# Kernel tuning notes

Measured on AMD Instinct MI355X. Metric: run time of the kernel, lower is better.

## Reference

```python
import jax, jax.numpy as jnp
import numpy as np

B, CIN, COUT, RES, WDIM, K, GRID = 2, 512, 512, 256, 512, 3, 8
W_COORD_DIST, W_LERP_MULT = 2.0, 1.0
LRELU_SLOPE = 0.2
ACT_GAIN = float(np.sqrt(2.0))  # bias_act def_gain for lrelu
PAD = K // 2  # force_zero_padding=False -> padding = kernel_size//2


def setup_inputs() -> dict:
    key = jax.random.key(0)
    ks = jax.random.split(key, 8)
    return {
        "x": jax.random.normal(ks[0], (B, CIN, RES, RES), jnp.float32),
        "w": jax.random.normal(ks[1], (B, WDIM), jnp.float32),
        "w_context": jax.random.normal(ks[2], (B, 2, WDIM), jnp.float32),
        "weight": jax.random.normal(ks[3], (COUT, CIN, K, K), jnp.float32),
        "affine_w": jax.random.normal(ks[4], (CIN, WDIM), jnp.float32),
        "affine_b": jnp.ones((CIN,), jnp.float32),  # bias_init=1
        "bias": jnp.zeros((COUT,), jnp.float32),
        "noise_strength": jnp.float32(0.1),  # nonzero so noise path is active
        "noise_raw": jax.random.normal(ks[5], (B, 1, RES, RES), jnp.float32),
        "left_borders_idx": jax.random.randint(ks[6], (B,), 0, GRID),
    }


def _to_patches(x):
    # [b,c,h,w] -> [b*grid, c, h, w/grid], matching view/permute order in patchwise_op
    b, c, h, w = x.shape
    wp = w // GRID
    return x.reshape(b, c, h, GRID, wp).transpose(0, 3, 1, 2, 4).reshape(b * GRID, c, h, wp)


def _from_patches(y, b):
    bg, c, h, wp = y.shape
    return y.reshape(b, GRID, c, h, wp).transpose(0, 2, 3, 1, 4).reshape(b, c, h, GRID * wp)


def _style_lerp(x, styles, left_borders_idx):
    # fast_manual_bilinear_mult_row: width-wise piecewise-linear interpolation of
    # 3 style anchors (left ctx, center, right ctx); center anchor sits at the
    # column given by left_borders_idx (in patch units); anchor spacing = w*w_coord_dist/2.
    b, c, h, w = x.shape
    patch = w // GRID
    D = w * W_COORD_DIST / 2.0
    cols = jnp.arange(w, dtype=x.dtype) + 0.5  # [w]
    center = left_borders_idx.astype(x.dtype)[:, None] * patch  # [b,1]
    t = jnp.clip((cols[None, :] - center) / D * W_LERP_MULT, -1.0, 1.0)  # [b,w]
    a = jnp.clip(-t, 0.0, 1.0)   # weight on left-context style
    r = jnp.clip(t, 0.0, 1.0)    # weight on right-context style
    m = 1.0 - a - r              # weight on center style
    scol = (a[..., None] * styles[:, 0][:, None, :]
            + m[..., None] * styles[:, 1][:, None, :]
            + r[..., None] * styles[:, 2][:, None, :])  # [b,w,c]
    return x * scol.transpose(0, 2, 1)[:, :, None, :]  # broadcast over h


def reference(x, w, w_context, weight, affine_w, affine_b, bias, noise_strength, noise_raw, left_borders_idx):
    b = x.shape[0]
    # run_spatial_affine: FullyConnectedLayer with weight_gain 1/sqrt(w_dim)
    wg = jnp.stack([w_context[:, 0], w, w_context[:, 1]], axis=1)  # [b,3,wdim]
    styles = jnp.einsum('bsd,cd->bsc', wg, affine_w) * (1.0 / np.sqrt(WDIM)) + affine_b  # [b,3,cin]

    # per-patch instance norm (unbiased std over (h, w_patch)), h > grid*2 holds
    wp = RES // GRID
    xp = x.reshape(b, CIN, RES, GRID, wp)
    std = jnp.std(xp, axis=(2, 4), keepdims=True, ddof=1)
    x = (xp / (std + 1e-8)).reshape(b, CIN, RES, RES)

    # style modulation
    x = _style_lerp(x, styles, left_borders_idx)

    # patchwise conv2d (up=1, flip_weight=True -> plain cross-correlation, pad k//2)
    xpat = _to_patches(x)
    y = jax.lax.conv_general_dilated(
        xpat, weight, window_strides=(1, 1), padding=((PAD, PAD), (PAD, PAD)),
        dimension_numbers=('NCHW', 'OIHW', 'NCHW'))
    x = _from_patches(y, b)

    # demodulation + noise fma
    demod = jax.lax.rsqrt(jnp.sum(weight * weight, axis=(1, 2, 3)) + 1e-8)  # [cout]
    x = x * demod[None, :, None, None] + noise_raw * noise_strength

    # bias_act: lrelu(x+b) * def_gain (gain=1, no clamp)
    x = x + bias[None, :, None, None]
    return jnp.where(x >= 0, x, x * LRELU_SLOPE) * ACT_GAIN
```

## Files before the change

### kernel.cpp

```cpp
#include <hip/hip_runtime.h>
#include <hip/hip_bf16.h>

#define BATCH 2
#define CIN 512
#define COUT 512
#define RES 256
#define WDIM 512
#define GRIDP 8
#define PW 32
#define NPATCH 16
#define LRELU 0.2f
#define ACT_GAIN 1.41421356237309515f

typedef __attribute__((ext_vector_type(8))) short bf16x8;
typedef __attribute__((ext_vector_type(4))) float f32x4;

#define SZ_XMOD (134217728ULL)
#define OFF_WBF (SZ_XMOD)
#define SZ_WBF  (9ULL*512*512*2)
#define OFF_STYLES (OFF_WBF + SZ_WBF)
#define SZ_STYLES (2*3*512*4)
#define OFF_INVSTD (OFF_STYLES + SZ_STYLES)
#define SZ_INVSTD (2*512*8*4)
#define OFF_DEMOD (OFF_INVSTD + SZ_INVSTD)

__global__ void k_styles(const float* __restrict__ w, const float* __restrict__ wctx,
                         const float* __restrict__ affw, const float* __restrict__ affb,
                         float* __restrict__ styles) {
    int tid = blockIdx.x * 256 + threadIdx.x;
    if (tid >= BATCH * 3 * CIN) return;
    int c = tid & 511;
    int s = (tid >> 9) % 3;
    int b = tid / (3 * 512);
    const float* row = (s == 0) ? (wctx + b * 2 * WDIM)
                     : (s == 1) ? (w + b * WDIM)
                                : (wctx + b * 2 * WDIM + WDIM);
    const float* aw = affw + (size_t)c * WDIM;
    float acc = 0.f;
    for (int d = 0; d < WDIM; ++d) acc += row[d] * aw[d];
    styles[tid] = acc * 0.044194173824159216f + affb[c];
}

__global__ void k_wprep(const float* __restrict__ weight, __hip_bfloat16* __restrict__ wbf,
                        float* __restrict__ demod) {
    int o = blockIdx.x;
    int t = threadIdx.x;
    const float* wrow = weight + (size_t)o * 4608;
    float ss = 0.f;
    for (int i = t; i < 4608; i += 256) { float v = wrow[i]; ss += v * v; }
    #pragma unroll
    for (int off = 32; off; off >>= 1) ss += __shfl_down(ss, off, 64);
    __shared__ float red[4];
    if ((t & 63) == 0) red[t >> 6] = ss;
    __syncthreads();
    if (t == 0) {
        float tot = red[0] + red[1] + red[2] + red[3];
        demod[o] = 1.0f / sqrtf(tot + 1e-8f);
    }
    for (int k = 0; k < 9; ++k)
        for (int ci = t; ci < 512; ci += 256)
            wbf[(size_t)k * COUT * CIN + (size_t)o * CIN + ci] = __float2bfloat16(wrow[ci * 9 + k]);
}

__global__ void k_std(const float* __restrict__ x, float* __restrict__ inv_std) {
    int bid = blockIdx.x;
    int g = bid & 7;
    int c = (bid >> 3) & 511;
    int b = bid >> 12;
    const float* base = x + ((size_t)(b * 512 + c) * 256) * 256 + g * 32;
    int t = threadIdx.x;
    float s = 0.f, ss = 0.f;
    #pragma unroll 4
    for (int i = 0; i < 32; ++i) {
        int e = t + (i << 8);
        int h = e >> 5, wp = e & 31;
        float v = base[h * 256 + wp];
        s += v; ss += v * v;
    }
    #pragma unroll
    for (int off = 32; off; off >>= 1) {
        s += __shfl_down(s, off, 64);
        ss += __shfl_down(ss, off, 64);
    }
    __shared__ float rs[4], rss[4];
    if ((t & 63) == 0) { rs[t >> 6] = s; rss[t >> 6] = ss; }
    __syncthreads();
    if (t == 0) {
        float S = rs[0] + rs[1] + rs[2] + rs[3];
        float SS = rss[0] + rss[1] + rss[2] + rss[3];
        float var = (SS - S * S * (1.f / 8192.f)) * (1.f / 8191.f);
        var = fmaxf(var, 0.f);
        inv_std[bid] = 1.f / (sqrtf(var) + 1e-8f);
    }
}

__global__ void k_normmod(const float* __restrict__ x, const float* __restrict__ styles,
                          const float* __restrict__ inv_std, const int* __restrict__ lbi,
                          __hip_bfloat16* __restrict__ xmod) {
    int bid = blockIdx.x;
    int ht = bid & 31;
    int cc = (bid >> 5) & 7;
    int p = bid >> 8;
    int b = p >> 3, g = p & 7;
    int t = threadIdx.x;
    __shared__ float st[3][64];
    __shared__ float istd[64];
    __shared__ __align__(16) __hip_bfloat16 tile[8 * 33 * 66];
    if (t < 192) {
        int s = t / 64, c = t % 64;
        st[s][c] = styles[(b * 3 + s) * 512 + cc * 64 + c];
    } else {
        int c = t - 192;
        istd[c] = inv_std[(b * 512 + cc * 64 + c) * 8 + g];
    }
    __syncthreads();
    float center = (float)(lbi[b] * PW);
    const float* xb = x + ((size_t)(b * 512 + cc * 64) * 256 + ht * 8) * 256 + g * 32;
    #pragma unroll 4
    for (int i = 0; i < 16; ++i) {
        int cell = t + (i << 8);
        int c = cell >> 6;
        int rem = cell & 63;
        int h = rem >> 3;
        int v4 = rem & 7;
        float4 xv = *(const float4*)(xb + ((size_t)c * 256 + h) * 256 + v4 * 4);
        float sc = istd[c];
        float s0 = st[0][c], s1 = st[1][c], s2 = st[2][c];
        float colb = (float)(g * 32 + v4 * 4) + 0.5f;
        const float* xvp = &xv.x;
        #pragma unroll
        for (int k = 0; k < 4; ++k) {
            float tc = (colb + (float)k - center) * 0.00390625f;
            tc = fminf(fmaxf(tc, -1.f), 1.f);
            float a = fmaxf(-tc, 0.f), r = fmaxf(tc, 0.f);
            float m = 1.f - a - r;
            float scol = a * s0 + m * s1 + r * s2;
            tile[(h * 33 + (v4 * 4 + k)) * 66 + c] = __float2bfloat16(xvp[k] * sc * scol);
        }
    }
    __syncthreads();
    __hip_bfloat16* ob = xmod + (size_t)(p * 256 + ht * 8) * 32 * 512 + cc * 64;
    #pragma unroll 4
    for (int i = 0; i < 8; ++i) {
        int cell = t + (i << 8);
        int c8 = cell & 7;
        int wp = (cell >> 3) & 31;
        int h = cell >> 8;
        const __hip_bfloat16* src = tile + (h * 33 + wp) * 66 + c8 * 8;
        uint4 v;
        v.x = *(const unsigned*)(src);
        v.y = *(const unsigned*)(src + 2);
        v.z = *(const unsigned*)(src + 4);
        v.w = *(const unsigned*)(src + 6);
        *(uint4*)(ob + (size_t)(h * 32 + wp) * 512 + c8 * 8) = v;
    }
}

__global__ void __launch_bounds__(256, 2)
k_conv(const __hip_bfloat16* __restrict__ xmod, const __hip_bfloat16* __restrict__ wbf,
       const float* __restrict__ demod, const float* __restrict__ bias,
       const float* __restrict__ noise, const float* __restrict__ nstr_p,
       float* __restrict__ out) {
    int ht = blockIdx.x;
    int p = blockIdx.y;
    int mb = blockIdx.z;
    int b = p >> 3, g = p & 7;
    int cout0 = mb * 128;
    int h0b = ht * 4;
    int t = threadIdx.x;
    int lane = t & 63, wid = t >> 6;
    int wm = wid >> 1, wn = wid & 1;
    int l15 = lane & 15, q = lane >> 4;

    __shared__ __align__(16) __hip_bfloat16 wsA[3 * 128 * 32];
    __shared__ __align__(16) __hip_bfloat16 xsB[4 * 6 * 34 * 8];

    f32x4 acc[4][4];
    #pragma unroll
    for (int i = 0; i < 4; ++i)
        #pragma unroll
        for (int j = 0; j < 4; ++j) acc[i][j] = (f32x4){0.f, 0.f, 0.f, 0.f};

    const __hip_bfloat16* xpat = xmod + (size_t)p * 256 * 32 * 512;

    for (int cin0 = 0; cin0 < 512; cin0 += 32) {
        __syncthreads();
        for (int idx = t; idx < 816; idx += 256) {
            int k8 = idx / 204;
            int rem = idx - k8 * 204;
            int hs = rem / 34;
            int wps = rem - hs * 34;
            int hg = h0b + hs - 1;
            uint4 v = make_uint4(0u, 0u, 0u, 0u);
            if (wps >= 1 && wps <= 32 && hg >= 0 && hg < 256)
                v = *(const uint4*)(xpat + (size_t)(hg * 32 + (wps - 1)) * 512 + cin0 + k8 * 8);
            *(uint4*)(xsB + ((k8 * 6 + hs) * 34 + wps) * 8) = v;
        }
        for (int kh = 0; kh < 3; ++kh) {
            __syncthreads();
            for (int idx = t; idx < 1536; idx += 256) {
                int kw = idx >> 9;
                int r = (idx >> 2) & 127;
                int k8 = idx & 3;
                uint4 v = *(const uint4*)(wbf + (size_t)((kh * 3 + kw) * 512 + cout0 + r) * 512 + cin0 + k8 * 8);
                *(uint4*)(wsA + ((kw * 128 + r) * 32 + k8 * 8)) = v;
            }
            __syncthreads();
            #pragma unroll
            for (int kw = 0; kw < 3; ++kw) {
                bf16x8 af[4], bfr[4];
                #pragma unroll
                for (int mf = 0; mf < 4; ++mf)
                    af[mf] = *(const bf16x8*)(wsA + ((kw * 128 + wm * 64 + mf * 16 + l15) * 32 + q * 8));
                #pragma unroll
                for (int j = 0; j < 4; ++j) {
                    int hl = wn * 2 + (j >> 1);
                    int wp0 = (j & 1) * 16;
                    bfr[j] = *(const bf16x8*)(xsB + ((q * 6 + hl + kh) * 34 + wp0 + kw + l15) * 8);
                }
                #pragma unroll
                for (int mf = 0; mf < 4; ++mf)
                    #pragma unroll
                    for (int j = 0; j < 4; ++j)
                        acc[mf][j] = __builtin_amdgcn_mfma_f32_16x16x32_bf16(af[mf], bfr[j], acc[mf][j], 0, 0, 0);
            }
        }
    }

    float nstr = nstr_p[0];
    #pragma unroll
    for (int j = 0; j < 4; ++j) {
        int hl = wn * 2 + (j >> 1);
        int hg = h0b + hl;
        int colg = g * 32 + (j & 1) * 16 + l15;
        float nv = noise[(size_t)b * 65536 + hg * 256 + colg] * nstr;
        #pragma unroll
        for (int mf = 0; mf < 4; ++mf) {
            int cbase = cout0 + wm * 64 + mf * 16 + q * 4;
            #pragma unroll
            for (int r = 0; r < 4; ++r) {
                int c = cbase + r;
                float v = acc[mf][j][r] * demod[c] + nv + bias[c];
                v = (v >= 0.f ? v : v * LRELU) * ACT_GAIN;
                out[((size_t)(b * 512 + c) * 256 + hg) * 256 + colg] = v;
            }
        }
    }
}

extern "C" void kernel_launch(void* const* d_in, const int* in_sizes, int n_in,
                              void* d_out, int out_size, void* d_ws, size_t ws_size,
                              hipStream_t stream) {
    const float* x      = (const float*)d_in[0];
    const float* w      = (const float*)d_in[1];
    const float* wctx   = (const float*)d_in[2];
    const float* weight = (const float*)d_in[3];
    const float* affw   = (const float*)d_in[4];
    const float* affb   = (const float*)d_in[5];
    const float* bias   = (const float*)d_in[6];
    const float* nstr   = (const float*)d_in[7];
    const float* noise  = (const float*)d_in[8];
    const int*   lbi    = (const int*)d_in[9];
    float* out = (float*)d_out;

    char* wsb = (char*)d_ws;
    __hip_bfloat16* xmod = (__hip_bfloat16*)wsb;
    __hip_bfloat16* wbf  = (__hip_bfloat16*)(wsb + OFF_WBF);
    float* styles        = (float*)(wsb + OFF_STYLES);
    float* invstd        = (float*)(wsb + OFF_INVSTD);
    float* demod         = (float*)(wsb + OFF_DEMOD);

    k_styles<<<12, 256, 0, stream>>>(w, wctx, affw, affb, styles);
    k_wprep<<<512, 256, 0, stream>>>(weight, wbf, demod);
    k_std<<<8192, 256, 0, stream>>>(x, invstd);
    k_normmod<<<4096, 256, 0, stream>>>(x, styles, invstd, lbi, xmod);
    k_conv<<<dim3(64, 16, 4), 256, 0, stream>>>(xmod, wbf, demod, bias, noise, nstr, out);
}
```

Measured before the change: 1.424 ms.

## Double-buffer weight tiles via direct global-to-LDS loads and enlarge conv tile

Restructures the implicit-GEMM conv kernel so each block covers 8 output rows and each wave computes all 128 output channels for two rows (8x4 MFMA accumulators). Weight tiles are double-buffered in LDS and loaded with global_load_lds, with an XOR swizzle to avoid bank conflicts. Activations for the next cin slice are prefetched into registers while the current slice computes. This reduces barrier count, global reload redundancy and load latency exposure, at the cost of higher register pressure (128 accumulator floats) and more LDS, which may lower occupancy under launch_bounds(256,2).

```diff
diff --git a/kernel.cpp b/kernel.cpp
--- a/kernel.cpp
+++ b/kernel.cpp
@@ -23,6 +23,10 @@
 #define OFF_INVSTD (OFF_STYLES + SZ_STYLES)
 #define SZ_INVSTD (2*512*8*4)
 #define OFF_DEMOD (OFF_INVSTD + SZ_INVSTD)
+
+#define GLOAD16(gp, lp) __builtin_amdgcn_global_load_lds( \
+    (const __attribute__((address_space(1))) void*)(gp),  \
+    (__attribute__((address_space(3))) void*)(lp), 16, 0, 0)
 
 __global__ void k_styles(const float* __restrict__ w, const float* __restrict__ wctx,
                          const float* __restrict__ affw, const float* __restrict__ affb,
@@ -161,86 +165,143 @@
        const float* __restrict__ demod, const float* __restrict__ bias,
        const float* __restrict__ noise, const float* __restrict__ nstr_p,
        float* __restrict__ out) {
-    int ht = blockIdx.x;
-    int p = blockIdx.y;
-    int mb = blockIdx.z;
-    int b = p >> 3, g = p & 7;
-    int cout0 = mb * 128;
-    int h0b = ht * 4;
-    int t = threadIdx.x;
-    int lane = t & 63, wid = t >> 6;
-    int wm = wid >> 1, wn = wid & 1;
-    int l15 = lane & 15, q = lane >> 4;
-
-    __shared__ __align__(16) __hip_bfloat16 wsA[3 * 128 * 32];
-    __shared__ __align__(16) __hip_bfloat16 xsB[4 * 6 * 34 * 8];
-
-    f32x4 acc[4][4];
-    #pragma unroll
-    for (int i = 0; i < 4; ++i)
-        #pragma unroll
-        for (int j = 0; j < 4; ++j) acc[i][j] = (f32x4){0.f, 0.f, 0.f, 0.f};
+    const int ht = blockIdx.x;
+    const int p  = blockIdx.y;
+    const int mb = blockIdx.z;
+    const int b = p >> 3, g = p & 7;
+    const int cout0 = mb * 128;
+    const int h0b = ht * 8;
+    const int t = threadIdx.x;
+    const int lane = t & 63, wid = t >> 6;
+    const int l15 = lane & 15, q = lane >> 4;
+    const int sw = (l15 >> 1) & 3;
+    const int qs = q ^ sw;
+
+    __shared__ __align__(16) __hip_bfloat16 wsA[2 * 3 * 128 * 32];
+    __shared__ __align__(16) __hip_bfloat16 xsB[4 * 10 * 34 * 8];
+
+    int xgo[6]; int xlo[6]; bool xin[6]; bool xld[6];
+    #pragma unroll
+    for (int i = 0; i < 6; ++i) {
+        int idx = t + i * 256;
+        int k8 = idx / 340;
+        int rem = idx - k8 * 340;
+        int hs = rem / 34;
+        int wps = rem - hs * 34;
+        int hg = h0b + hs - 1;
+        xin[i] = idx < 1360;
+        xld[i] = xin[i] && (wps >= 1) && (wps <= 32) && (hg >= 0) && (hg < 256);
+        xgo[i] = (hg * 32 + (wps - 1)) * 512 + k8 * 8;
+        xlo[i] = ((k8 * 10 + hs) * 34 + wps) * 8;
+    }
+
+    int wgo[6];
+    #pragma unroll
+    for (int i = 0; i < 6; ++i) {
+        int idx = (wid * 6 + i) * 64 + lane;
+        int kw = idx >> 9;
+        int r  = (idx >> 2) & 127;
+        int c4 = idx & 3;
+        int k8 = c4 ^ ((r >> 1) & 3);
+        wgo[i] = kw * 262144 + (cout0 + r) * 512 + k8 * 8;
+    }
 
     const __hip_bfloat16* xpat = xmod + (size_t)p * 256 * 32 * 512;
-
+    const __hip_bfloat16* xb = xsB + ((q * 10 + wid * 2) * 34 + l15) * 8;
+
+    f32x4 acc[8][4];
+    #pragma unroll
+    for (int mf = 0; mf < 8; ++mf)
+        #pragma unroll
+        for (int j = 0; j < 4; ++j) acc[mf][j] = (f32x4){0.f, 0.f, 0.f, 0.f};
+
+    uint4 xw[6];
+    #pragma unroll
+    for (int i = 0; i < 6; ++i) {
+        uint4 v = make_uint4(0u, 0u, 0u, 0u);
+        if (xld[i]) v = *(const uint4*)(xpat + xgo[i]);
+        xw[i] = v;
+    }
+    {
+        __hip_bfloat16* ldst = wsA + wid * 6 * 512;
+        #pragma unroll
+        for (int i = 0; i < 6; ++i)
+            GLOAD16(wbf + wgo[i], ldst + i * 512);
+    }
+
+    int pb = 0;
     for (int cin0 = 0; cin0 < 512; cin0 += 32) {
-        __syncthreads();
-        for (int idx = t; idx < 816; idx += 256) {
-            int k8 = idx / 204;
-            int rem = idx - k8 * 204;
-            int hs = rem / 34;
-            int wps = rem - hs * 34;
-            int hg = h0b + hs - 1;
-            uint4 v = make_uint4(0u, 0u, 0u, 0u);
-            if (wps >= 1 && wps <= 32 && hg >= 0 && hg < 256)
-                v = *(const uint4*)(xpat + (size_t)(hg * 32 + (wps - 1)) * 512 + cin0 + k8 * 8);
-            *(uint4*)(xsB + ((k8 * 6 + hs) * 34 + wps) * 8) = v;
-        }
+        #pragma unroll
         for (int kh = 0; kh < 3; ++kh) {
-            __syncthreads();
-            for (int idx = t; idx < 1536; idx += 256) {
-                int kw = idx >> 9;
-                int r = (idx >> 2) & 127;
-                int k8 = idx & 3;
-                uint4 v = *(const uint4*)(wbf + (size_t)((kh * 3 + kw) * 512 + cout0 + r) * 512 + cin0 + k8 * 8);
-                *(uint4*)(wsA + ((kw * 128 + r) * 32 + k8 * 8)) = v;
-            }
-            __syncthreads();
+            asm volatile("s_waitcnt vmcnt(0) lgkmcnt(0)" ::: "memory");
+            __builtin_amdgcn_s_barrier();
+
+            if (kh == 0) {
+                #pragma unroll
+                for (int i = 0; i < 6; ++i)
+                    if (xin[i]) *(uint4*)(xsB + xlo[i]) = xw[i];
+            }
+            if (!((cin0 == 480) && (kh == 2))) {
+                int nkh  = (kh == 2) ? 0 : kh + 1;
+                int ncin = (kh == 2) ? cin0 + 32 : cin0;
+                const __hip_bfloat16* wsrc = wbf + nkh * 786432 + ncin;
+                __hip_bfloat16* ldst = wsA + (pb ^ 1) * 12288 + wid * 6 * 512;
+                #pragma unroll
+                for (int i = 0; i < 6; ++i)
+                    GLOAD16(wsrc + wgo[i], ldst + i * 512);
+            }
+            if (kh == 0) {
+                asm volatile("s_waitcnt lgkmcnt(0)" ::: "memory");
+                __builtin_amdgcn_s_barrier();
+            }
+            if (kh == 2 && cin0 < 480) {
+                #pragma unroll
+                for (int i = 0; i < 6; ++i) {
+                    uint4 v = make_uint4(0u, 0u, 0u, 0u);
+                    if (xld[i]) v = *(const uint4*)(xpat + xgo[i] + cin0 + 32);
+                    xw[i] = v;
+                }
+            }
+
+            const __hip_bfloat16* wb = wsA + pb * 12288 + l15 * 32 + qs * 8;
             #pragma unroll
             for (int kw = 0; kw < 3; ++kw) {
-                bf16x8 af[4], bfr[4];
-                #pragma unroll
-                for (int mf = 0; mf < 4; ++mf)
-                    af[mf] = *(const bf16x8*)(wsA + ((kw * 128 + wm * 64 + mf * 16 + l15) * 32 + q * 8));
+                bf16x8 af[8];
+                #pragma unroll
+                for (int mf = 0; mf < 8; ++mf)
+                    af[mf] = *(const bf16x8*)(wb + kw * 4096 + mf * 512);
                 #pragma unroll
                 for (int j = 0; j < 4; ++j) {
-                    int hl = wn * 2 + (j >> 1);
-                    int wp0 = (j & 1) * 16;
-                    bfr[j] = *(const bf16x8*)(xsB + ((q * 6 + hl + kh) * 34 + wp0 + kw + l15) * 8);
+                    bf16x8 bj = *(const bf16x8*)(xb + (((j >> 1) + kh) * 34 + (j & 1) * 16 + kw) * 8);
+                    #pragma unroll
+                    for (int mf = 0; mf < 8; ++mf)
+                        acc[mf][j] = __builtin_amdgcn_mfma_f32_16x16x32_bf16(af[mf], bj, acc[mf][j], 0, 0, 0);
                 }
-                #pragma unroll
-                for (int mf = 0; mf < 4; ++mf)
-                    #pragma unroll
-                    for (int j = 0; j < 4; ++j)
-                        acc[mf][j] = __builtin_amdgcn_mfma_f32_16x16x32_bf16(af[mf], bfr[j], acc[mf][j], 0, 0, 0);
-            }
+            }
+            pb ^= 1;
         }
     }
 
     float nstr = nstr_p[0];
+    float nv[4];
     #pragma unroll
     for (int j = 0; j < 4; ++j) {
-        int hl = wn * 2 + (j >> 1);
-        int hg = h0b + hl;
+        int hg = h0b + wid * 2 + (j >> 1);
         int colg = g * 32 + (j & 1) * 16 + l15;
-        float nv = noise[(size_t)b * 65536 + hg * 256 + colg] * nstr;
-        #pragma unroll
-        for (int mf = 0; mf < 4; ++mf) {
-            int cbase = cout0 + wm * 64 + mf * 16 + q * 4;
+        nv[j] = noise[(size_t)b * 65536 + hg * 256 + colg] * nstr;
+    }
+    #pragma unroll
+    for (int mf = 0; mf < 8; ++mf) {
+        #pragma unroll
+        for (int r = 0; r < 4; ++r) {
+            int c = cout0 + mf * 16 + q * 4 + r;
+            float dm = demod[c];
+            float bi = bias[c];
             #pragma unroll
-            for (int r = 0; r < 4; ++r) {
-                int c = cbase + r;
-                float v = acc[mf][j][r] * demod[c] + nv + bias[c];
+            for (int j = 0; j < 4; ++j) {
+                int hg = h0b + wid * 2 + (j >> 1);
+                int colg = g * 32 + (j & 1) * 16 + l15;
+                float v = acc[mf][j][r] * dm + nv[j] + bi;
                 v = (v >= 0.f ? v : v * LRELU) * ACT_GAIN;
                 out[((size_t)(b * 512 + c) * 256 + hg) * 256 + colg] = v;
             }
@@ -274,5 +335,5 @@
     k_wprep<<<512, 256, 0, stream>>>(weight, wbf, demod);
     k_std<<<8192, 256, 0, stream>>>(x, invstd);
     k_normmod<<<4096, 256, 0, stream>>>(x, styles, invstd, lbi, xmod);
-    k_conv<<<dim3(64, 16, 4), 256, 0, stream>>>(xmod, wbf, demod, bias, noise, nstr, out);
-}
+    k_conv<<<dim3(32, 16, 4), 256, 0, stream>>>(xmod, wbf, demod, bias, noise, nstr, out);
+}
```

Result: faster. 1.394 ms (-2.1%).
